# Optimization experiments

Hardware: AMD Instinct MI355X
Metric: run time of the kernel (lower is better)

Reference implementation:

```python
import jax, jax.numpy as jnp
import numpy as np

SLOPE = 15.0

@jax.custom_vjp
def spike_fn(x):
    return (x > 0).astype(x.dtype)

def _spike_fwd(x):
    return (x > 0).astype(x.dtype), x

def _spike_bwd(x, g):
    # fast_sigmoid surrogate: d/dx = 1 / (slope*|x| + 1)^2
    return (g / (SLOPE * jnp.abs(x) + 1.0) ** 2,)

spike_fn.defvjp(_spike_fwd, _spike_bwd)

def setup_inputs() -> dict:
    key = jax.random.key(0)
    ks = jax.random.split(key, 8)
    B, T, C = 256, 500, 700
    x = jax.random.uniform(ks[0], (B, T, C), dtype=jnp.float32)
    def lin(k, fan_in, fan_out):
        kw, kb = jax.random.split(k)
        bound = 1.0 / np.sqrt(fan_in)
        W = jax.random.uniform(kw, (fan_out, fan_in), minval=-bound, maxval=bound, dtype=jnp.float32)
        b = jax.random.uniform(kb, (fan_out,), minval=-bound, maxval=bound, dtype=jnp.float32)
        return W, b
    W1, b1 = lin(ks[1], C, 128)
    W2, b2 = lin(ks[2], 128, 256)
    W3, b3 = lin(ks[3], 256, 20)
    beta = jnp.float32(0.8)
    thr = jnp.float32(1.0)
    return {"x": x, "W1": W1, "b1": b1, "W2": W2, "b2": b2, "W3": W3, "b3": b3,
            "beta1": beta, "beta2": beta, "beta3": beta,
            "thr1": thr, "thr2": thr, "thr3": thr}

def _lif(mem, cur, beta, thr):
    # snntorch Leaky, reset_mechanism='subtract': reset from previous mem (detached)
    reset = jax.lax.stop_gradient((mem - thr > 0).astype(mem.dtype))
    mem = jnp.clip(beta, 0.0, 1.0) * mem + cur - reset * thr
    spk = spike_fn(mem - thr)
    return spk, mem

def reference(x, W1, b1, W2, b2, W3, b3, beta1, beta2, beta3, thr1, thr2, thr3):
    B, T, C = x.shape
    xt = jnp.swapaxes(x, 0, 1)  # [T, B, C]

    def step(carry, x_t):
        m1, m2, m3 = carry
        cur1 = x_t @ W1.T + b1
        s1, m1 = _lif(m1, cur1, beta1, thr1)
        cur2 = s1 @ W2.T + b2
        s2, m2 = _lif(m2, cur2, beta2, thr2)
        cur3 = s2 @ W3.T + b3
        s3, m3 = _lif(m3, cur3, beta3, thr3)
        return (m1, m2, m3), s3

    init = (jnp.zeros((B, 128), x.dtype), jnp.zeros((B, 256), x.dtype), jnp.zeros((B, 20), x.dtype))
    _, spk3 = jax.lax.scan(step, init, xt)  # [T, B, 20]
    return spk3.mean(axis=0)  # [B, 20]
```

## Files before the change

kernel.cpp:

```cpp
#include <hip/hip_runtime.h>

typedef __attribute__((ext_vector_type(8))) short short8;
typedef __attribute__((ext_vector_type(4))) float f32x4;

#define MFMA16(a, b, c) __builtin_amdgcn_mfma_f32_16x16x32_bf16(a, b, c, 0, 0, 0)

__device__ __forceinline__ ushort bf16_rne(float f) {
  uint u = __float_as_uint(f);
  u += 0x7FFFu + ((u >> 16) & 1u);
  return (ushort)(u >> 16);
}

__device__ __forceinline__ void gload_lds16(const void* g, void* l) {
  __builtin_amdgcn_global_load_lds((const __attribute__((address_space(1))) uint*)g,
                                   (__attribute__((address_space(3))) uint*)l, 16, 0, 0);
}

__global__ void split_w_kernel(const float* __restrict__ W, ushort* __restrict__ hi,
                               ushort* __restrict__ lo, int Nr, int K, int Npad, int Kp) {
  int i = blockIdx.x * 256 + threadIdx.x;
  if (i >= Npad * Kp) return;
  int r = i / Kp, k = i - r * Kp;
  float v = (r < Nr && k < K) ? W[(size_t)r * K + k] : 0.f;
  ushort h = bf16_rne(v);
  float hf = __uint_as_float(((uint)h) << 16);
  ushort l = bf16_rne(v - hf);
  hi[i] = h;
  lo[i] = l;
}

__global__ __launch_bounds__(256, 3) void gemm1_kernel(const float* __restrict__ A,
                                                       const ushort* __restrict__ Bh,
                                                       const ushort* __restrict__ Bl,
                                                       float* __restrict__ C) {
  __shared__ ushort sAh[64 * 64];
  __shared__ ushort sAl[64 * 64];
  __shared__ ushort sBh[128 * 64];
  __shared__ ushort sBl[128 * 64];

  const int tid = threadIdx.x;
  const int lane = tid & 63;
  const int wid = tid >> 6;
  const int tr = tid >> 2, tg = tid & 3;
  const int wr = wid >> 1, wc = wid & 1;
  const int m0 = blockIdx.x * 64;

  const int brow_lo = lane >> 3;
  const int bswz = (((lane & 7) ^ brow_lo) << 3);
  const size_t bgoff = (size_t)(wid * 32 + brow_lo) * 704 + bswz;

  f32x4 acc[2][4];
#pragma unroll
  for (int i = 0; i < 2; ++i)
#pragma unroll
    for (int j = 0; j < 4; ++j) acc[i][j] = f32x4{0.f, 0.f, 0.f, 0.f};

  float4 pf[4];
  auto load_a = [&](int ks) {
    const float* ap = A + (size_t)(m0 + tr) * 700 + ks * 64 + tg * 16;
#pragma unroll
    for (int q = 0; q < 4; ++q) {
      float4 z;
      z.x = z.y = z.z = z.w = 0.f;
      pf[q] = (ks * 64 + tg * 16 + q * 4 + 3 < 700) ? *(const float4*)(ap + q * 4) : z;
    }
  };
  load_a(0);

  for (int ks = 0; ks < 11; ++ks) {
#pragma unroll
    for (int p = 0; p < 4; ++p) {
      const size_t go = bgoff + (size_t)p * 8 * 704 + ks * 64;
      gload_lds16(Bh + go, &sBh[(wid * 32 + p * 8) * 64]);
      gload_lds16(Bl + go, &sBl[(wid * 32 + p * 8) * 64]);
    }
#pragma unroll
    for (int h = 0; h < 2; ++h) {
      const float* vf = (const float*)&pf[h * 2];
      uint hw[4], lw[4];
#pragma unroll
      for (int q = 0; q < 4; ++q) {
        const uint u0 = __float_as_uint(vf[2 * q]);
        const uint u1 = __float_as_uint(vf[2 * q + 1]);
        hw[q] = __builtin_amdgcn_perm(u1, u0, 0x07060302u);
        const float d0 = vf[2 * q] - __uint_as_float(u0 & 0xFFFF0000u);
        const float d1 = vf[2 * q + 1] - __uint_as_float(u1 & 0xFFFF0000u);
        asm("v_cvt_pk_bf16_f32 %0, %1, %2" : "=v"(lw[q]) : "v"(d0), "v"(d1));
      }
      const int off = tr * 64 + (((tg * 2 + h) ^ (tr & 7)) << 3);
      uint4 qh, ql;
      qh.x = hw[0]; qh.y = hw[1]; qh.z = hw[2]; qh.w = hw[3];
      ql.x = lw[0]; ql.y = lw[1]; ql.z = lw[2]; ql.w = lw[3];
      *(uint4*)&sAh[off] = qh;
      *(uint4*)&sAl[off] = ql;
    }
    __syncthreads();
    if (ks < 10) load_a(ks + 1);

#pragma unroll
    for (int ku = 0; ku < 2; ++ku) {
      const int g0 = ku * 4 + (lane >> 4);
      short8 ah[2], al[2];
#pragma unroll
      for (int i = 0; i < 2; ++i) {
        const int r = wr * 32 + i * 16 + (lane & 15);
        const int off = r * 64 + ((g0 ^ (r & 7)) << 3);
        ah[i] = *(const short8*)&sAh[off];
        al[i] = *(const short8*)&sAl[off];
      }
      short8 bh[4], bl[4];
#pragma unroll
      for (int j = 0; j < 4; ++j) {
        const int r = wc * 64 + j * 16 + (lane & 15);
        const int off = r * 64 + ((g0 ^ (r & 7)) << 3);
        bh[j] = *(const short8*)&sBh[off];
        bl[j] = *(const short8*)&sBl[off];
      }
#pragma unroll
      for (int i = 0; i < 2; ++i)
#pragma unroll
        for (int j = 0; j < 4; ++j) {
          acc[i][j] = MFMA16(ah[i], bh[j], acc[i][j]);
          acc[i][j] = MFMA16(al[i], bh[j], acc[i][j]);
          acc[i][j] = MFMA16(ah[i], bl[j], acc[i][j]);
        }
    }
    __syncthreads();
  }

#pragma unroll
  for (int i = 0; i < 2; ++i) {
    const int rbase = m0 + wr * 32 + i * 16 + ((lane >> 4) << 2);
#pragma unroll
    for (int j = 0; j < 4; ++j) {
      const int col = wc * 64 + j * 16 + (lane & 15);
#pragma unroll
      for (int rg = 0; rg < 4; ++rg)
        C[(size_t)(rbase + rg) * 128 + col] = acc[i][j][rg];
    }
  }
}

__global__ __launch_bounds__(512, 2) void fused_l23_kernel(
    const float* __restrict__ cur1, const float* __restrict__ b1,
    const ushort* __restrict__ w2h, const ushort* __restrict__ w2l, const float* __restrict__ b2,
    const ushort* __restrict__ w3h, const ushort* __restrict__ w3l, const float* __restrict__ b3,
    const float* __restrict__ beta1p, const float* __restrict__ beta2p,
    const float* __restrict__ beta3p, const float* __restrict__ thr1p,
    const float* __restrict__ thr2p, const float* __restrict__ thr3p,
    float* __restrict__ out) {
  __shared__ __align__(16) char smem[156672];
  float* buf = (float*)smem;
  ushort* s1 = (ushort*)(smem + 32768);
  float* c2 = (float*)(smem + 49152);
  ushort* s2 = (ushort*)(smem + 49152);
  ushort* w3p = (ushort*)(smem + 114688);
  float* c3 = (float*)(smem + 147456);

  const int tid = threadIdx.x;
  const int lane = tid & 63;
  const int w = tid >> 6;
  const int b = blockIdx.x;
  const int lr = lane & 15, lg = lane >> 4;

  const float be1 = fminf(fmaxf(beta1p[0], 0.f), 1.f), th1 = thr1p[0];
  const float be2 = fminf(fmaxf(beta2p[0], 0.f), 1.f), th2 = thr2p[0];
  const float be3 = fminf(fmaxf(beta3p[0], 0.f), 1.f), th3 = thr3p[0];
  const float bi1 = (tid < 128) ? b1[tid] : 0.f;
  const float bi2 = (tid < 256) ? b2[tid] : 0.f;
  const float bi3 = (tid >= 128 && tid < 148) ? b3[tid - 128] : 0.f;

  short8 w2fh[2][4], w2fl[2][4];
#pragma unroll
  for (int j = 0; j < 2; ++j)
#pragma unroll
    for (int ks = 0; ks < 4; ++ks) {
      const size_t o = (size_t)(w * 32 + j * 16 + lr) * 128 + ks * 32 + lg * 8;
      w2fh[j][ks] = *(const short8*)(w2h + o);
      w2fl[j][ks] = *(const short8*)(w2l + o);
    }
#pragma unroll
  for (int p = 0; p < 2; ++p) {
    const int r = p * 16 + (tid >> 5);
    const int g = tid & 31;
    const int swz = ((g ^ (r & 7)) << 3);
    *(uint4*)&w3p[r * 256 + g * 8] = *(const uint4*)(w3h + r * 256 + swz);
    *(uint4*)&w3p[8192 + r * 256 + g * 8] = *(const uint4*)(w3l + r * 256 + swz);
  }
  const float4* cg4 = (const float4*)cur1 + (size_t)b * 16000;
#pragma unroll
  for (int i = 0; i < 4; ++i) ((float4*)buf)[i * 512 + tid] = cg4[i * 512 + tid];
  __syncthreads();

  float m1 = 0.f, m2 = 0.f, m3 = 0.f, a3 = 0.f;

  for (int c = 0; c < 8; ++c) {
    const int t0 = c * 64;

    if (tid < 128) {
      const int g = tid >> 3, nb = tid & 7;
#pragma unroll
      for (int hh = 0; hh < 2; ++hh) {
        float v[32];
#pragma unroll
        for (int u = 0; u < 32; ++u) v[u] = buf[(hh * 32 + u) * 128 + tid];
#pragma unroll
        for (int u = 0; u < 32; ++u) {
          const int row = hh * 32 + u;
          const int t = t0 + row;
          ushort sp = 0;
          if (t < 500) {
            float r = (m1 > th1) ? th1 : 0.f;
            m1 = be1 * m1 + (v[u] + bi1) - r;
            sp = (m1 > th1) ? (ushort)0x3F80 : (ushort)0;
          }
          s1[row * 128 + ((g ^ (row & 7)) << 3) + nb] = sp;
        }
      }
    } else if (tid < 148 && c > 0) {
      const int n = tid - 128;
      const int tp = (c - 1) * 64;
#pragma unroll 8
      for (int u = 0; u < 64; ++u) {
        if (tp + u < 500) {
          const float v = c3[u * 36 + n];
          float r = (m3 > th3) ? th3 : 0.f;
          m3 = be3 * m3 + (v + bi3) - r;
          a3 += (m3 > th3) ? 1.f : 0.f;
        }
      }
    }
    __syncthreads();

    {
      f32x4 acc[4][2];
#pragma unroll
      for (int i = 0; i < 4; ++i)
#pragma unroll
        for (int j = 0; j < 2; ++j) acc[i][j] = f32x4{0.f, 0.f, 0.f, 0.f};
#pragma unroll
      for (int ks = 0; ks < 4; ++ks) {
        const int G = ks * 4 + lg;
        short8 ah[4];
#pragma unroll
        for (int i = 0; i < 4; ++i) {
          const int r = i * 16 + lr;
          ah[i] = *(const short8*)&s1[r * 128 + ((G ^ (r & 7)) << 3)];
        }
#pragma unroll
        for (int j = 0; j < 2; ++j)
#pragma unroll
          for (int i = 0; i < 4; ++i) {
            acc[i][j] = MFMA16(ah[i], w2fh[j][ks], acc[i][j]);
            acc[i][j] = MFMA16(ah[i], w2fl[j][ks], acc[i][j]);
          }
      }
#pragma unroll
      for (int i = 0; i < 4; ++i) {
        const int rbase = i * 16 + (lg << 2);
#pragma unroll
        for (int j = 0; j < 2; ++j) {
          const int col = w * 32 + j * 16 + lr;
#pragma unroll
          for (int rg = 0; rg < 4; ++rg) {
            const int row = rbase + rg;
            c2[row * 256 + (col ^ ((row & 7) << 2))] = acc[i][j][rg];
          }
        }
      }
    }
    __syncthreads();

    float v[32];
    if (tid < 256) {
#pragma unroll
      for (int u = 0; u < 32; ++u) v[u] = c2[u * 256 + (tid ^ ((u & 7) << 2))];
    } else if (c < 7) {
      const int base = (c + 1) * 2048;
#pragma unroll
      for (int i = 0; i < 8; ++i)
        ((float4*)buf)[i * 256 + (tid - 256)] = cg4[base + i * 256 + (tid - 256)];
    }
    __syncthreads();

    if (tid < 256) {
      const int g = tid >> 3, nb = tid & 7;
#pragma unroll
      for (int u = 0; u < 32; ++u) {
        const int t = t0 + u;
        ushort sp = 0;
        if (t < 500) {
          float r = (m2 > th2) ? th2 : 0.f;
          m2 = be2 * m2 + (v[u] + bi2) - r;
          sp = (m2 > th2) ? (ushort)0x3F80 : (ushort)0;
        }
        s2[u * 256 + ((g ^ (u & 7)) << 3) + nb] = sp;
      }
#pragma unroll
      for (int u = 0; u < 32; ++u) v[u] = c2[(32 + u) * 256 + (tid ^ ((u & 7) << 2))];
#pragma unroll
      for (int u = 0; u < 32; ++u) {
        const int row = 32 + u;
        const int t = t0 + row;
        ushort sp = 0;
        if (t < 500) {
          float r = (m2 > th2) ? th2 : 0.f;
          m2 = be2 * m2 + (v[u] + bi2) - r;
          sp = (m2 > th2) ? (ushort)0x3F80 : (ushort)0;
        }
        s2[row * 256 + ((g ^ (row & 7)) << 3) + nb] = sp;
      }
    }
    __syncthreads();

    {
      const int wr3 = w >> 1, wc3 = w & 1;
      f32x4 a3c = f32x4{0.f, 0.f, 0.f, 0.f};
#pragma unroll
      for (int ku = 0; ku < 8; ++ku) {
        const int G = ku * 4 + lg;
        const int rb = wc3 * 16 + lr;
        const int ob = rb * 256 + ((G ^ (rb & 7)) << 3);
        short8 vbh = *(const short8*)&w3p[ob];
        short8 vbl = *(const short8*)&w3p[8192 + ob];
        const int r = wr3 * 16 + lr;
        short8 av = *(const short8*)&s2[r * 256 + ((G ^ (r & 7)) << 3)];
        a3c = MFMA16(av, vbh, a3c);
        a3c = MFMA16(av, vbl, a3c);
      }
      const int rb3 = wr3 * 16 + (lg << 2);
      const int col3 = wc3 * 16 + lr;
#pragma unroll
      for (int rg = 0; rg < 4; ++rg) c3[(rb3 + rg) * 36 + col3] = a3c[rg];
    }
    __syncthreads();
  }

  if (tid >= 128 && tid < 148) {
    const int n = tid - 128;
#pragma unroll 8
    for (int u = 0; u < 64; ++u) {
      if (448 + u < 500) {
        const float v = c3[u * 36 + n];
        float r = (m3 > th3) ? th3 : 0.f;
        m3 = be3 * m3 + (v + bi3) - r;
        a3 += (m3 > th3) ? 1.f : 0.f;
      }
    }
    out[(size_t)b * 20 + n] = a3 * (1.f / 500.f);
  }
}

extern "C" void kernel_launch(void* const* d_in, const int* in_sizes, int n_in, void* d_out,
                              int out_size, void* d_ws, size_t ws_size, hipStream_t stream) {
  const float* x = (const float*)d_in[0];
  const float* W1 = (const float*)d_in[1];
  const float* b1 = (const float*)d_in[2];
  const float* W2 = (const float*)d_in[3];
  const float* b2 = (const float*)d_in[4];
  const float* W3 = (const float*)d_in[5];
  const float* b3 = (const float*)d_in[6];
  const float* beta1 = (const float*)d_in[7];
  const float* beta2 = (const float*)d_in[8];
  const float* beta3 = (const float*)d_in[9];
  const float* thr1 = (const float*)d_in[10];
  const float* thr2 = (const float*)d_in[11];
  const float* thr3 = (const float*)d_in[12];
  float* out = (float*)d_out;

  const int M = 128000;
  char* ws = (char*)d_ws;
  float* cur1 = (float*)ws;
  size_t off = (size_t)M * 128 * 4;
  ushort* w1h = (ushort*)(ws + off); off += 128 * 704 * 2;
  ushort* w1l = (ushort*)(ws + off); off += 128 * 704 * 2;
  ushort* w2h = (ushort*)(ws + off); off += 256 * 128 * 2;
  ushort* w2l = (ushort*)(ws + off); off += 256 * 128 * 2;
  ushort* w3h = (ushort*)(ws + off); off += 32 * 256 * 2;
  ushort* w3l = (ushort*)(ws + off); off += 32 * 256 * 2;

  split_w_kernel<<<(128 * 704 + 255) / 256, 256, 0, stream>>>(W1, w1h, w1l, 128, 700, 128, 704);
  split_w_kernel<<<(256 * 128 + 255) / 256, 256, 0, stream>>>(W2, w2h, w2l, 256, 128, 256, 128);
  split_w_kernel<<<(32 * 256 + 255) / 256, 256, 0, stream>>>(W3, w3h, w3l, 20, 256, 32, 256);

  gemm1_kernel<<<M / 64, 256, 0, stream>>>(x, w1h, w1l, cur1);
  fused_l23_kernel<<<256, 512, 0, stream>>>(cur1, b1, w2h, w2l, b2, w3h, w3l, b3,
                                            beta1, beta2, beta3, thr1, thr2, thr3, out);
}
```

Baseline: 188.7 us.

## Double-buffer GEMM1 LDS tiles with 512 threads and merge weight split kernels

The x@W1 GEMM now double-buffers its A and B tiles in shared memory, staging the next K-slice while MFMAs run on the current one, and prefetches A two steps ahead. The block grows to 512 threads (8 waves in a 2x4 layout), so each wave computes a 32x32 tile instead of 32x64. The three weight-splitting kernels are merged into one launch. LDS use doubles to about 96KB and occupancy is limited to one block per CU, which may reduce latency hiding across blocks.

```diff
diff --git a/kernel.cpp b/kernel.cpp
--- a/kernel.cpp
+++ b/kernel.cpp
@@ -16,10 +16,24 @@
                                    (__attribute__((address_space(3))) uint*)l, 16, 0, 0);
 }
 
-__global__ void split_w_kernel(const float* __restrict__ W, ushort* __restrict__ hi,
-                               ushort* __restrict__ lo, int Nr, int K, int Npad, int Kp) {
+__global__ void split_w_all_kernel(const float* __restrict__ W1, ushort* __restrict__ w1h,
+                                   ushort* __restrict__ w1l, const float* __restrict__ W2,
+                                   ushort* __restrict__ w2h, ushort* __restrict__ w2l,
+                                   const float* __restrict__ W3, ushort* __restrict__ w3h,
+                                   ushort* __restrict__ w3l) {
   int i = blockIdx.x * 256 + threadIdx.x;
-  if (i >= Npad * Kp) return;
+  const float* W;
+  ushort *hi, *lo;
+  int Nr, K, Kp;
+  if (i < 128 * 704) {
+    W = W1; hi = w1h; lo = w1l; Nr = 128; K = 700; Kp = 704;
+  } else if (i < 128 * 704 + 256 * 128) {
+    i -= 128 * 704;
+    W = W2; hi = w2h; lo = w2l; Nr = 256; K = 128; Kp = 128;
+  } else {
+    i -= 128 * 704 + 256 * 128;
+    W = W3; hi = w3h; lo = w3l; Nr = 20; K = 256; Kp = 256;
+  }
   int r = i / Kp, k = i - r * Kp;
   float v = (r < Nr && k < K) ? W[(size_t)r * K + k] : 0.f;
   ushort h = bf16_rne(v);
@@ -29,97 +43,105 @@
   lo[i] = l;
 }
 
-__global__ __launch_bounds__(256, 3) void gemm1_kernel(const float* __restrict__ A,
+__global__ __launch_bounds__(512, 1) void gemm1_kernel(const float* __restrict__ A,
                                                        const ushort* __restrict__ Bh,
                                                        const ushort* __restrict__ Bl,
                                                        float* __restrict__ C) {
-  __shared__ ushort sAh[64 * 64];
-  __shared__ ushort sAl[64 * 64];
-  __shared__ ushort sBh[128 * 64];
-  __shared__ ushort sBl[128 * 64];
+  __shared__ ushort sAh[2][64 * 64];
+  __shared__ ushort sAl[2][64 * 64];
+  __shared__ ushort sBh[2][128 * 64];
+  __shared__ ushort sBl[2][128 * 64];
 
   const int tid = threadIdx.x;
   const int lane = tid & 63;
-  const int wid = tid >> 6;
-  const int tr = tid >> 2, tg = tid & 3;
-  const int wr = wid >> 1, wc = wid & 1;
+  const int w = tid >> 6;
+  const int wr = w >> 2, wc = w & 3;
   const int m0 = blockIdx.x * 64;
-
-  const int brow_lo = lane >> 3;
-  const int bswz = (((lane & 7) ^ brow_lo) << 3);
-  const size_t bgoff = (size_t)(wid * 32 + brow_lo) * 704 + bswz;
-
-  f32x4 acc[2][4];
+  const int ar = tid >> 3, ag = tid & 7;
+
+  const int br8 = lane >> 3;
+  const int bswz = (((lane & 7) ^ br8) << 3);
+
+  f32x4 acc[2][2];
 #pragma unroll
   for (int i = 0; i < 2; ++i)
 #pragma unroll
-    for (int j = 0; j < 4; ++j) acc[i][j] = f32x4{0.f, 0.f, 0.f, 0.f};
-
-  float4 pf[4];
+    for (int j = 0; j < 2; ++j) acc[i][j] = f32x4{0.f, 0.f, 0.f, 0.f};
+
+  float4 pf[2];
   auto load_a = [&](int ks) {
-    const float* ap = A + (size_t)(m0 + tr) * 700 + ks * 64 + tg * 16;
+    const int k = ks * 64 + ag * 8;
+    const float* ap = A + (size_t)(m0 + ar) * 700 + k;
+    float4 z;
+    z.x = z.y = z.z = z.w = 0.f;
+    pf[0] = (k + 3 < 700) ? *(const float4*)ap : z;
+    pf[1] = (k + 7 < 700) ? *(const float4*)(ap + 4) : z;
+  };
+  auto stage_b = [&](int ks, int buf) {
+#pragma unroll
+    for (int round = 0; round < 2; ++round) {
+      const int rbase = w * 16 + round * 8;
+      const size_t go = (size_t)(rbase + br8) * 704 + ks * 64 + bswz;
+      gload_lds16(Bh + go, &sBh[buf][rbase * 64]);
+      gload_lds16(Bl + go, &sBl[buf][rbase * 64]);
+    }
+  };
+  auto stage_a = [&](int buf) {
+    const float vf[8] = {pf[0].x, pf[0].y, pf[0].z, pf[0].w, pf[1].x, pf[1].y, pf[1].z, pf[1].w};
+    uint hw[4], lw[4];
 #pragma unroll
     for (int q = 0; q < 4; ++q) {
-      float4 z;
-      z.x = z.y = z.z = z.w = 0.f;
-      pf[q] = (ks * 64 + tg * 16 + q * 4 + 3 < 700) ? *(const float4*)(ap + q * 4) : z;
-    }
+      const uint u0 = __float_as_uint(vf[2 * q]);
+      const uint u1 = __float_as_uint(vf[2 * q + 1]);
+      hw[q] = __builtin_amdgcn_perm(u1, u0, 0x07060302u);
+      const float d0 = vf[2 * q] - __uint_as_float(u0 & 0xFFFF0000u);
+      const float d1 = vf[2 * q + 1] - __uint_as_float(u1 & 0xFFFF0000u);
+      asm("v_cvt_pk_bf16_f32 %0, %1, %2" : "=v"(lw[q]) : "v"(d0), "v"(d1));
+    }
+    const int off = ar * 64 + ((ag ^ (ar & 7)) << 3);
+    uint4 qh, ql;
+    qh.x = hw[0]; qh.y = hw[1]; qh.z = hw[2]; qh.w = hw[3];
+    ql.x = lw[0]; ql.y = lw[1]; ql.z = lw[2]; ql.w = lw[3];
+    *(uint4*)&sAh[buf][off] = qh;
+    *(uint4*)&sAl[buf][off] = ql;
   };
+
   load_a(0);
+  stage_b(0, 0);
+  stage_a(0);
+  load_a(1);
+  __syncthreads();
 
   for (int ks = 0; ks < 11; ++ks) {
-#pragma unroll
-    for (int p = 0; p < 4; ++p) {
-      const size_t go = bgoff + (size_t)p * 8 * 704 + ks * 64;
-      gload_lds16(Bh + go, &sBh[(wid * 32 + p * 8) * 64]);
-      gload_lds16(Bl + go, &sBl[(wid * 32 + p * 8) * 64]);
-    }
-#pragma unroll
-    for (int h = 0; h < 2; ++h) {
-      const float* vf = (const float*)&pf[h * 2];
-      uint hw[4], lw[4];
-#pragma unroll
-      for (int q = 0; q < 4; ++q) {
-        const uint u0 = __float_as_uint(vf[2 * q]);
-        const uint u1 = __float_as_uint(vf[2 * q + 1]);
-        hw[q] = __builtin_amdgcn_perm(u1, u0, 0x07060302u);
-        const float d0 = vf[2 * q] - __uint_as_float(u0 & 0xFFFF0000u);
-        const float d1 = vf[2 * q + 1] - __uint_as_float(u1 & 0xFFFF0000u);
-        asm("v_cvt_pk_bf16_f32 %0, %1, %2" : "=v"(lw[q]) : "v"(d0), "v"(d1));
-      }
-      const int off = tr * 64 + (((tg * 2 + h) ^ (tr & 7)) << 3);
-      uint4 qh, ql;
-      qh.x = hw[0]; qh.y = hw[1]; qh.z = hw[2]; qh.w = hw[3];
-      ql.x = lw[0]; ql.y = lw[1]; ql.z = lw[2]; ql.w = lw[3];
-      *(uint4*)&sAh[off] = qh;
-      *(uint4*)&sAl[off] = ql;
-    }
-    __syncthreads();
-    if (ks < 10) load_a(ks + 1);
+    const int cur = ks & 1;
+    if (ks < 10) {
+      stage_b(ks + 1, 1 - cur);
+      stage_a(1 - cur);
+    }
+    if (ks < 9) load_a(ks + 2);
 
 #pragma unroll
     for (int ku = 0; ku < 2; ++ku) {
       const int g0 = ku * 4 + (lane >> 4);
-      short8 ah[2], al[2];
+      short8 ah[2], al[2], bh[2], bl[2];
 #pragma unroll
       for (int i = 0; i < 2; ++i) {
         const int r = wr * 32 + i * 16 + (lane & 15);
         const int off = r * 64 + ((g0 ^ (r & 7)) << 3);
-        ah[i] = *(const short8*)&sAh[off];
-        al[i] = *(const short8*)&sAl[off];
-      }
-      short8 bh[4], bl[4];
-#pragma unroll
-      for (int j = 0; j < 4; ++j) {
-        const int r = wc * 64 + j * 16 + (lane & 15);
+        ah[i] = *(const short8*)&sAh[cur][off];
+        al[i] = *(const short8*)&sAl[cur][off];
+      }
+#pragma unroll
+      for (int j = 0; j < 2; ++j) {
+        const int r = wc * 32 + j * 16 + (lane & 15);
         const int off = r * 64 + ((g0 ^ (r & 7)) << 3);
-        bh[j] = *(const short8*)&sBh[off];
-        bl[j] = *(const short8*)&sBl[off];
+        bh[j] = *(const short8*)&sBh[cur][off];
+        bl[j] = *(const short8*)&sBl[cur][off];
       }
 #pragma unroll
       for (int i = 0; i < 2; ++i)
 #pragma unroll
-        for (int j = 0; j < 4; ++j) {
+        for (int j = 0; j < 2; ++j) {
           acc[i][j] = MFMA16(ah[i], bh[j], acc[i][j]);
           acc[i][j] = MFMA16(al[i], bh[j], acc[i][j]);
           acc[i][j] = MFMA16(ah[i], bl[j], acc[i][j]);
@@ -132,8 +154,8 @@
   for (int i = 0; i < 2; ++i) {
     const int rbase = m0 + wr * 32 + i * 16 + ((lane >> 4) << 2);
 #pragma unroll
-    for (int j = 0; j < 4; ++j) {
-      const int col = wc * 64 + j * 16 + (lane & 15);
+    for (int j = 0; j < 2; ++j) {
+      const int col = wc * 32 + j * 16 + (lane & 15);
 #pragma unroll
       for (int rg = 0; rg < 4; ++rg)
         C[(size_t)(rbase + rg) * 128 + col] = acc[i][j][rg];
@@ -379,11 +401,9 @@
   ushort* w3h = (ushort*)(ws + off); off += 32 * 256 * 2;
   ushort* w3l = (ushort*)(ws + off); off += 32 * 256 * 2;
 
-  split_w_kernel<<<(128 * 704 + 255) / 256, 256, 0, stream>>>(W1, w1h, w1l, 128, 700, 128, 704);
-  split_w_kernel<<<(256 * 128 + 255) / 256, 256, 0, stream>>>(W2, w2h, w2l, 256, 128, 256, 128);
-  split_w_kernel<<<(32 * 256 + 255) / 256, 256, 0, stream>>>(W3, w3h, w3l, 20, 256, 32, 256);
-
-  gemm1_kernel<<<M / 64, 256, 0, stream>>>(x, w1h, w1l, cur1);
+  split_w_all_kernel<<<512, 256, 0, stream>>>(W1, w1h, w1l, W2, w2h, w2l, W3, w3h, w3l);
+
+  gemm1_kernel<<<M / 64, 512, 0, stream>>>(x, w1h, w1l, cur1);
   fused_l23_kernel<<<256, 512, 0, stream>>>(cur1, b1, w2h, w2l, b2, w3h, w3l, b3,
                                             beta1, beta2, beta3, thr1, thr2, thr3, out);
 }
```

Measured after the change: 214.2 us. 13.6% more time.
